# Optimization experiments

Measured on AMD Instinct MI355X. Metric: run time of the kernel, lower is better.

## Reference

```python
import jax, jax.numpy as jnp
import numpy as np

N, E, HID, H = 20000, 200000, 96, 6
HC = H * HID  # 576


def _ln(x, g, b):
    mu = x.mean(-1, keepdims=True)
    v = ((x - mu) ** 2).mean(-1, keepdims=True)
    return (x - mu) / jnp.sqrt(v + 1e-5) * g + b


def _gatv2(x, edge_emb, src, dst, Wl, bl, Wr, br, We, attw, cbias):
    # PyG GATv2Conv, concat=False, edge_dim=HID, eval mode (no dropout)
    xl = (x @ Wl + bl).reshape(N, H, HID)   # source transform (lin_l)
    xr = (x @ Wr + br).reshape(N, H, HID)   # target transform (lin_r)
    ee = (edge_emb @ We).reshape(E, H, HID) # lin_edge (no bias in PyG)
    h = jax.nn.leaky_relu(xl[src] + xr[dst] + ee, 0.2)   # [E,H,C]
    logits = jnp.einsum('ehc,hc->eh', h, attw)            # [E,H]
    m = jax.ops.segment_max(logits, dst, num_segments=N)  # segment softmax over dst
    ex = jnp.exp(logits - m[dst])
    den = jax.ops.segment_sum(ex, dst, num_segments=N)
    alpha = ex / (den[dst] + 1e-16)
    out = jax.ops.segment_sum(xl[src] * alpha[..., None], dst, num_segments=N)  # [N,H,C]
    return out.mean(axis=1) + cbias  # concat=False -> head mean, then bias


def _forward(x, edge_attr, ne_w, ne_b, ne_g, ne_beta, ee_w, ee_b, ee_g, ee_beta,
             Wl, bl, Wr, br, We, attw, cbias, lng, lnb,
             p1_w, p1_b, p1_g, p1_beta, p2_w, p2_b, p2_g, p2_beta, p3_w, p3_b,
             edge_index):
    src, dst = edge_index[0], edge_index[1]
    x = jax.nn.relu(_ln(x @ ne_w + ne_b, ne_g, ne_beta))
    edge_emb = jax.nn.relu(_ln(edge_attr @ ee_w + ee_b, ee_g, ee_beta))
    for i in range(3):  # fixed small layer count
        h = _gatv2(x, edge_emb, src, dst, Wl[i], bl[i], Wr[i], br[i], We[i], attw[i], cbias[i])
        if i < 2:
            h = jax.nn.elu(h)
        x = x + _ln(h, lng[i], lnb[i])
    ctx = jnp.concatenate([x[src], x[dst], edge_emb], axis=1)  # [E, 3*HID]
    h = jax.nn.relu(_ln(ctx @ p1_w + p1_b, p1_g, p1_beta))
    h = jax.nn.relu(_ln(h @ p2_w + p2_b, p2_g, p2_beta))
    return h @ p3_w + p3_b  # [E,1]


def setup_inputs():
    key = jax.random.key(0)
    ks = jax.random.split(key, 16)
    g = lambda k, shape, s: jax.random.normal(k, shape, dtype=jnp.float32) * s
    inp = {}
    inp['x'] = g(ks[0], (N, 4), 1.0)
    inp['edge_attr'] = g(ks[1], (E, 3), 1.0)
    inp['edge_index'] = jax.random.randint(ks[2], (2, E), 0, N, dtype=jnp.int32)
    # encoders
    inp['ne_w'] = g(ks[3], (4, HID), 0.5); inp['ne_b'] = jnp.zeros((HID,), jnp.float32)
    inp['ne_g'] = jnp.ones((HID,), jnp.float32); inp['ne_beta'] = jnp.zeros((HID,), jnp.float32)
    inp['ee_w'] = g(ks[4], (3, HID), 0.5); inp['ee_b'] = jnp.zeros((HID,), jnp.float32)
    inp['ee_g'] = jnp.ones((HID,), jnp.float32); inp['ee_beta'] = jnp.zeros((HID,), jnp.float32)
    # 3 stacked GATv2 layers
    inp['Wl'] = g(ks[5], (3, HID, HC), 0.1); inp['bl'] = jnp.zeros((3, HC), jnp.float32)
    inp['Wr'] = g(ks[6], (3, HID, HC), 0.1); inp['br'] = jnp.zeros((3, HC), jnp.float32)
    inp['We'] = g(ks[7], (3, HID, HC), 0.1)
    inp['attw'] = g(ks[8], (3, H, HID), 0.1)
    inp['cbias'] = jnp.zeros((3, HID), jnp.float32)
    inp['lng'] = jnp.ones((3, HID), jnp.float32); inp['lnb'] = jnp.zeros((3, HID), jnp.float32)
    # predictor MLP
    inp['p1_w'] = g(ks[9], (3 * HID, 128), 0.1); inp['p1_b'] = jnp.zeros((128,), jnp.float32)
    inp['p1_g'] = jnp.ones((128,), jnp.float32); inp['p1_beta'] = jnp.zeros((128,), jnp.float32)
    inp['p2_w'] = g(ks[10], (128, 64), 0.1); inp['p2_b'] = jnp.zeros((64,), jnp.float32)
    inp['p2_g'] = jnp.ones((64,), jnp.float32); inp['p2_beta'] = jnp.zeros((64,), jnp.float32)
    inp['p3_w'] = g(ks[11], (64, 1), 0.1); inp['p3_b'] = jnp.zeros((1,), jnp.float32)
    return inp


def reference(x, edge_attr, edge_index, ne_w, ne_b, ne_g, ne_beta, ee_w, ee_b, ee_g, ee_beta,
              Wl, bl, Wr, br, We, attw, cbias, lng, lnb,
              p1_w, p1_b, p1_g, p1_beta, p2_w, p2_b, p2_g, p2_beta, p3_w, p3_b):
    return _forward(x, edge_attr, ne_w, ne_b, ne_g, ne_beta, ee_w, ee_b, ee_g, ee_beta,
                    Wl, bl, Wr, br, We, attw, cbias, lng, lnb,
                    p1_w, p1_b, p1_g, p1_beta, p2_w, p2_b, p2_g, p2_beta, p3_w, p3_b,
                    edge_index)
```

## Files before the change

kernel.cpp:

```cpp
#include <hip/hip_runtime.h>
#include <math.h>

#define NN 20000
#define NE 200000

typedef __attribute__((ext_vector_type(8))) short bf16x8;
typedef __attribute__((ext_vector_type(8))) unsigned short u16x8;
typedef __attribute__((ext_vector_type(4))) float f32x4;

__device__ __forceinline__ unsigned short f2bf(float x) {
  union { float f; unsigned u; } c; c.f = x;
  unsigned r = c.u + 0x7FFF + ((c.u >> 16) & 1);
  return (unsigned short)(r >> 16);
}
__device__ __forceinline__ float bf2f(unsigned short u) {
  union { unsigned u; float f; } c; c.u = ((unsigned)u) << 16;
  return c.f;
}

template <int D>
__global__ __launch_bounds__(256) void encode_row_kernel(
    const float* __restrict__ in,
    const float* __restrict__ W, const float* __restrict__ b,
    const float* __restrict__ g, const float* __restrict__ beta,
    float* __restrict__ out, unsigned short* __restrict__ outb, int R) {
  int row = blockIdx.x * 256 + threadIdx.x;
  if (row >= R) return;
  float vin[D];
#pragma unroll
  for (int k = 0; k < D; k++) vin[k] = in[(size_t)row * D + k];
  float y[96];
  float s = 0.f, s2 = 0.f;
#pragma unroll
  for (int j = 0; j < 96; j++) {
    float v = b[j];
#pragma unroll
    for (int k = 0; k < D; k++) v += vin[k] * W[k * 96 + j];
    y[j] = v;
    s += v;
    s2 += v * v;
  }
  float mu = s * (1.f / 96.f);
  float var = s2 * (1.f / 96.f) - mu * mu;
  float rs = rsqrtf(var + 1e-5f);
#pragma unroll
  for (int c = 0; c < 12; c++) {
    u16x8 pk;
    float yo[8];
#pragma unroll
    for (int j = 0; j < 8; j++) {
      int jj = c * 8 + j;
      float v = (y[jj] - mu) * rs * g[jj] + beta[jj];
      v = fmaxf(v, 0.f);
      yo[j] = v;
      pk[j] = f2bf(v);
    }
    *(u16x8*)&outb[(size_t)row * 96 + c * 8] = pk;
    if (out) {
      f32x4 o0 = {yo[0], yo[1], yo[2], yo[3]};
      f32x4 o1 = {yo[4], yo[5], yo[6], yo[7]};
      *(f32x4*)&out[(size_t)row * 96 + c * 8] = o0;
      *(f32x4*)&out[(size_t)row * 96 + c * 8 + 4] = o1;
    }
  }
}

__global__ void convW_kernel(const float* __restrict__ We,
                             unsigned short* __restrict__ WeTb,
                             const float* __restrict__ Wl,
                             unsigned short* __restrict__ WlTb,
                             const float* __restrict__ Wr,
                             unsigned short* __restrict__ WrTb,
                             const float* __restrict__ p1w,
                             unsigned short* __restrict__ p1wT,
                             const float* __restrict__ p2w,
                             unsigned short* __restrict__ p2wT) {
  int idx = blockIdx.x * 256 + threadIdx.x;
  if (idx < 3 * 576 * 96) {
    int l = idx / (576 * 96);
    int rem = idx % (576 * 96);
    int n = rem / 96, k = rem % 96;
    size_t sidx = (size_t)l * 96 * 576 + (size_t)k * 576 + n;
    WeTb[idx] = f2bf(We[sidx]);
    WlTb[idx] = f2bf(Wl[sidx]);
    WrTb[idx] = f2bf(Wr[sidx]);
  }
  if (idx < 128 * 288) {
    int n = idx / 288, k = idx % 288;
    p1wT[idx] = f2bf(p1w[(size_t)k * 128 + n]);
  }
  if (idx < 64 * 128) {
    int n = idx / 128, k = idx % 128;
    p2wT[idx] = f2bf(p2w[(size_t)k * 64 + n]);
  }
}

__global__ void hist_kernel(const int* __restrict__ dst, int* __restrict__ deg) {
  int e = blockIdx.x * blockDim.x + threadIdx.x;
  if (e < NE) atomicAdd(&deg[dst[e]], 1);
}

__global__ __launch_bounds__(1024) void scan_kernel(
    const int* __restrict__ deg, int* __restrict__ rowptr, int* __restrict__ cursor) {
  __shared__ int wsum[16];
  int t = threadIdx.x;
  int base = t * 20;
  int loc[20];
  int s = 0;
#pragma unroll
  for (int j = 0; j < 20; j++) {
    int idx = base + j;
    int v = (idx < NN) ? deg[idx] : 0;
    loc[j] = s;
    s += v;
  }
  int lane = t & 63, wv = t >> 6;
  int inc = s;
#pragma unroll
  for (int off = 1; off < 64; off <<= 1) {
    int up = __shfl_up(inc, off);
    if (lane >= off) inc += up;
  }
  if (lane == 63) wsum[wv] = inc;
  __syncthreads();
  if (wv == 0) {
    int wval = (lane < 16) ? wsum[lane] : 0;
#pragma unroll
    for (int off = 1; off < 16; off <<= 1) {
      int up = __shfl_up(wval, off);
      if (lane >= off) wval += up;
    }
    if (lane < 16) wsum[lane] = wval;
  }
  __syncthreads();
  int wbase = (wv > 0) ? wsum[wv - 1] : 0;
  int excl = wbase + inc - s;
#pragma unroll
  for (int j = 0; j < 20; j++) {
    int idx = base + j;
    if (idx < NN) { rowptr[idx] = excl + loc[j]; cursor[idx] = excl + loc[j]; }
  }
  if (t == 0) rowptr[NN] = NE;
}

__global__ void scatter_kernel(const int* __restrict__ src,
                               const int* __restrict__ dst,
                               int* __restrict__ cursor, int* __restrict__ eidx,
                               int* __restrict__ srcp, int* __restrict__ dstp) {
  int e = blockIdx.x * blockDim.x + threadIdx.x;
  if (e < NE) {
    int d = dst[e];
    int p = atomicAdd(&cursor[d], 1);
    eidx[p] = e;
    srcp[p] = src[e];
    dstp[p] = d;
  }
}

__global__ __launch_bounds__(256) void xlxr_mfma_kernel(
    const unsigned short* __restrict__ Xb,
    const unsigned short* __restrict__ WlTb,
    const float* __restrict__ bl,
    const unsigned short* __restrict__ WrTb,
    const float* __restrict__ br,
    unsigned short* __restrict__ xlb, unsigned short* __restrict__ xrb) {
  int t = threadIdx.x;
  int wave = t >> 6, lane = t & 63;
  int l15 = lane & 15, quad = lane >> 4;
  int node = blockIdx.x * 64 + wave * 16 + l15;
  int nclamp = (node < NN) ? node : (NN - 1);
  bool valid = node < NN;
  const unsigned short* brow = &Xb[(size_t)nclamp * 96 + quad * 8];
  bf16x8 b0 = *(const bf16x8*)&brow[0];
  bf16x8 b1 = *(const bf16x8*)&brow[32];
  bf16x8 b2 = *(const bf16x8*)&brow[64];
#pragma unroll
  for (int mt = 0; mt < 36; mt++) {
    int wc = mt * 16 + l15;
    const unsigned short* aL = &WlTb[(size_t)wc * 96 + quad * 8];
    f32x4 accL = {0.f, 0.f, 0.f, 0.f};
    accL = __builtin_amdgcn_mfma_f32_16x16x32_bf16(*(const bf16x8*)&aL[0], b0, accL, 0, 0, 0);
    accL = __builtin_amdgcn_mfma_f32_16x16x32_bf16(*(const bf16x8*)&aL[32], b1, accL, 0, 0, 0);
    accL = __builtin_amdgcn_mfma_f32_16x16x32_bf16(*(const bf16x8*)&aL[64], b2, accL, 0, 0, 0);
    const unsigned short* aR = &WrTb[(size_t)wc * 96 + quad * 8];
    f32x4 accR = {0.f, 0.f, 0.f, 0.f};
    accR = __builtin_amdgcn_mfma_f32_16x16x32_bf16(*(const bf16x8*)&aR[0], b0, accR, 0, 0, 0);
    accR = __builtin_amdgcn_mfma_f32_16x16x32_bf16(*(const bf16x8*)&aR[32], b1, accR, 0, 0, 0);
    accR = __builtin_amdgcn_mfma_f32_16x16x32_bf16(*(const bf16x8*)&aR[64], b2, accR, 0, 0, 0);
    if (valid) {
      int c0 = mt * 16 + quad * 4;
      float4 bbL = *(const float4*)&bl[c0];
      float4 bbR = *(const float4*)&br[c0];
      ushort4 pL, pR;
      pL.x = f2bf(accL[0] + bbL.x); pL.y = f2bf(accL[1] + bbL.y);
      pL.z = f2bf(accL[2] + bbL.z); pL.w = f2bf(accL[3] + bbL.w);
      pR.x = f2bf(accR[0] + bbR.x); pR.y = f2bf(accR[1] + bbR.y);
      pR.z = f2bf(accR[2] + bbR.z); pR.w = f2bf(accR[3] + bbR.w);
      *(ushort4*)&xlb[(size_t)node * 576 + c0] = pL;
      *(ushort4*)&xrb[(size_t)node * 576 + c0] = pR;
    }
  }
}

__global__ __launch_bounds__(256) void logits_mfma_kernel(
    const unsigned short* __restrict__ EMBb,
    const unsigned short* __restrict__ WeTb,
    const float* __restrict__ attw,
    const unsigned short* __restrict__ XLb,
    const unsigned short* __restrict__ XRb,
    const int* __restrict__ eidx, const int* __restrict__ srcp,
    const int* __restrict__ dstp,
    float* __restrict__ logp) {
  __shared__ __align__(16) unsigned short emb[64][104];
  __shared__ __align__(16) unsigned short eeb[64][200];
  __shared__ int sd[64][2];
  int t = threadIdx.x;
  int p0 = blockIdx.x * 64;
  if (t < 128) sd[t >> 1][t & 1] = (t & 1) ? dstp[p0 + (t >> 1)] : srcp[p0 + (t >> 1)];
  {
    int e = t >> 2, c0 = (t & 3) * 24;
    int erow = eidx[p0 + e];
    const unsigned short* sp = &EMBb[(size_t)erow * 96 + c0];
    *(bf16x8*)&emb[e][c0]      = *(const bf16x8*)&sp[0];
    *(bf16x8*)&emb[e][c0 + 8]  = *(const bf16x8*)&sp[8];
    *(bf16x8*)&emb[e][c0 + 16] = *(const bf16x8*)&sp[16];
  }
  __syncthreads();

  int wave = t >> 6, lane = t & 63;
  int l15 = lane & 15, quad = lane >> 4;
  int el = t >> 2;
  int cq = (t & 3) * 24;
  int gsrc = sd[el][0];
  int gdst = sd[el][1];

  for (int hp = 0; hp < 3; hp++) {
    int h0 = hp * 2, h1 = hp * 2 + 1;
    const unsigned short* xl0 = &XLb[(size_t)gsrc * 576 + h0 * 96 + cq];
    const unsigned short* xr0 = &XRb[(size_t)gdst * 576 + h0 * 96 + cq];
    const unsigned short* xl1 = &XLb[(size_t)gsrc * 576 + h1 * 96 + cq];
    const unsigned short* xr1 = &XRb[(size_t)gdst * 576 + h1 * 96 + cq];
    bf16x8 gl0[3], gr0[3], gl1[3], gr1[3];
#pragma unroll
    for (int c8 = 0; c8 < 3; c8++) {
      gl0[c8] = *(const bf16x8*)&xl0[c8 * 8];
      gr0[c8] = *(const bf16x8*)&xr0[c8 * 8];
      gl1[c8] = *(const bf16x8*)&xl1[c8 * 8];
      gr1[c8] = *(const bf16x8*)&xr1[c8 * 8];
    }
#pragma unroll
    for (int k = 0; k < 3; k++) {
      int ntg = wave * 3 + k;
      int col = hp * 192 + ntg * 16 + l15;
      const unsigned short* brow = &WeTb[(size_t)col * 96 + quad * 8];
      bf16x8 b0 = *(const bf16x8*)&brow[0];
      bf16x8 b1 = *(const bf16x8*)&brow[32];
      bf16x8 b2 = *(const bf16x8*)&brow[64];
#pragma unroll
      for (int et = 0; et < 4; et++) {
        const unsigned short* ar = &emb[et * 16 + l15][quad * 8];
        bf16x8 a0 = *(const bf16x8*)&ar[0];
        bf16x8 a1 = *(const bf16x8*)&ar[32];
        bf16x8 a2 = *(const bf16x8*)&ar[64];
        f32x4 acc = {0.f, 0.f, 0.f, 0.f};
        acc = __builtin_amdgcn_mfma_f32_16x16x32_bf16(a0, b0, acc, 0, 0, 0);
        acc = __builtin_amdgcn_mfma_f32_16x16x32_bf16(a1, b1, acc, 0, 0, 0);
        acc = __builtin_amdgcn_mfma_f32_16x16x32_bf16(a2, b2, acc, 0, 0, 0);
#pragma unroll
        for (int r = 0; r < 4; r++)
          eeb[et * 16 + quad * 4 + r][ntg * 16 + l15] = f2bf(acc[r]);
      }
    }
    __syncthreads();
    float pl0 = 0.f, pl1 = 0.f;
    {
      const unsigned short* ee0 = &eeb[el][cq];
      const unsigned short* ee1 = &eeb[el][96 + cq];
      const f32x4* ap0 = (const f32x4*)&attw[h0 * 96 + cq];
      const f32x4* ap1 = (const f32x4*)&attw[h1 * 96 + cq];
#pragma unroll
      for (int c8 = 0; c8 < 3; c8++) {
        bf16x8 ev0 = *(const bf16x8*)&ee0[c8 * 8];
        bf16x8 ev1 = *(const bf16x8*)&ee1[c8 * 8];
        f32x4 a00 = ap0[c8 * 2], a01 = ap0[c8 * 2 + 1];
        f32x4 a10 = ap1[c8 * 2], a11 = ap1[c8 * 2 + 1];
#pragma unroll
        for (int j = 0; j < 4; j++) {
          float v0 = bf2f((unsigned short)ev0[j]) +
                     bf2f((unsigned short)gl0[c8][j]) +
                     bf2f((unsigned short)gr0[c8][j]);
          v0 = (v0 > 0.f) ? v0 : 0.2f * v0;
          pl0 += v0 * a00[j];
          float w0 = bf2f((unsigned short)ev0[j + 4]) +
                     bf2f((unsigned short)gl0[c8][j + 4]) +
                     bf2f((unsigned short)gr0[c8][j + 4]);
          w0 = (w0 > 0.f) ? w0 : 0.2f * w0;
          pl0 += w0 * a01[j];
          float v1 = bf2f((unsigned short)ev1[j]) +
                     bf2f((unsigned short)gl1[c8][j]) +
                     bf2f((unsigned short)gr1[c8][j]);
          v1 = (v1 > 0.f) ? v1 : 0.2f * v1;
          pl1 += v1 * a10[j];
          float w1 = bf2f((unsigned short)ev1[j + 4]) +
                     bf2f((unsigned short)gl1[c8][j + 4]) +
                     bf2f((unsigned short)gr1[c8][j + 4]);
          w1 = (w1 > 0.f) ? w1 : 0.2f * w1;
          pl1 += w1 * a11[j];
        }
      }
    }
    pl0 += __shfl_xor(pl0, 1); pl0 += __shfl_xor(pl0, 2);
    pl1 += __shfl_xor(pl1, 1); pl1 += __shfl_xor(pl1, 2);
    if ((t & 3) == 0) {
      size_t base = (size_t)(p0 + el) * 6 + hp * 2;
      logp[base] = pl0;
      logp[base + 1] = pl1;
    }
    __syncthreads();
  }
}

__global__ __launch_bounds__(256) void alpha_kernel(
    const float* __restrict__ logp, const int* __restrict__ rowptr,
    float* __restrict__ alpha) {
  int node = blockIdx.x * 4 + (threadIdx.x >> 6);
  int lane = threadIdx.x & 63;
  if (node >= NN) return;
  int r0 = rowptr[node], r1 = rowptr[node + 1];
  int d = r1 - r0;
  if (d == 0) return;
  if (d <= 64) {
    bool act = lane < d;
    int p = r0 + (act ? lane : (d - 1));
    float lg[6];
#pragma unroll
    for (int h = 0; h < 6; h++) lg[h] = logp[(size_t)p * 6 + h];
#pragma unroll
    for (int h = 0; h < 6; h++) {
      float m = act ? lg[h] : -1e30f;
#pragma unroll
      for (int off = 32; off > 0; off >>= 1) m = fmaxf(m, __shfl_xor(m, off));
      float w = act ? expf(lg[h] - m) : 0.f;
      float s = w;
#pragma unroll
      for (int off = 32; off > 0; off >>= 1) s += __shfl_xor(s, off);
      if (act) alpha[(size_t)p * 6 + h] = w / (s + 1e-16f);
    }
  } else {
    float m[6], s[6];
#pragma unroll
    for (int h = 0; h < 6; h++) { m[h] = -1e30f; s[h] = 0.f; }
    for (int cs = 0; cs < d; cs += 64) {
      int cnt = min(64, d - cs);
      bool act = lane < cnt;
      int p = r0 + cs + (act ? lane : (cnt - 1));
#pragma unroll
      for (int h = 0; h < 6; h++) {
        float lg = act ? logp[(size_t)p * 6 + h] : -1e30f;
        float cm = lg;
#pragma unroll
        for (int off = 32; off > 0; off >>= 1) cm = fmaxf(cm, __shfl_xor(cm, off));
        float newm = fmaxf(m[h], cm);
        float w = act ? expf(lg - newm) : 0.f;
        float ss = w;
#pragma unroll
        for (int off = 32; off > 0; off >>= 1) ss += __shfl_xor(ss, off);
        s[h] = s[h] * expf(m[h] - newm) + ss;
        m[h] = newm;
      }
    }
    float inv[6];
#pragma unroll
    for (int h = 0; h < 6; h++) inv[h] = 1.f / (s[h] + 1e-16f);
    for (int cs = 0; cs < d; cs += 64) {
      int cnt = min(64, d - cs);
      if (lane < cnt) {
        int p = r0 + cs + lane;
#pragma unroll
        for (int h = 0; h < 6; h++)
          alpha[(size_t)p * 6 + h] =
              expf(logp[(size_t)p * 6 + h] - m[h]) * inv[h];
      }
    }
  }
}

__global__ __launch_bounds__(576) void aggregate_kernel(
    float* __restrict__ x, unsigned short* __restrict__ xb,
    const unsigned short* __restrict__ XLb,
    const float* __restrict__ alpha, const int* __restrict__ rowptr,
    const int* __restrict__ srcp,
    const float* __restrict__ cbias, const float* __restrict__ lng,
    const float* __restrict__ lnb, int do_elu) {
  int n = blockIdx.x;
  int t = threadIdx.x;
  int r0 = rowptr[n];
  int d = rowptr[n + 1] - r0;
  __shared__ float scratch[576];
  __shared__ float fin[96];
  __shared__ float part[2][2];
  __shared__ float red[2];
  int wave = t >> 6, lane = t & 63;
  int h = t / 96;
  float acc = 0.f;
  int j = 0;
  for (; j + 4 <= d; j += 4) {
    int p = r0 + j;
    float w0 = alpha[(size_t)(p + 0) * 6 + h];
    float w1 = alpha[(size_t)(p + 1) * 6 + h];
    float w2 = alpha[(size_t)(p + 2) * 6 + h];
    float w3 = alpha[(size_t)(p + 3) * 6 + h];
    int s0 = srcp[p + 0], s1 = srcp[p + 1];
    int s2 = srcp[p + 2], s3 = srcp[p + 3];
    float x0 = bf2f(XLb[(size_t)s0 * 576 + t]);
    float x1 = bf2f(XLb[(size_t)s1 * 576 + t]);
    float x2 = bf2f(XLb[(size_t)s2 * 576 + t]);
    float x3 = bf2f(XLb[(size_t)s3 * 576 + t]);
    acc += w0 * x0 + w1 * x1 + w2 * x2 + w3 * x3;
  }
  for (; j < d; j++) {
    int p = r0 + j;
    acc += alpha[(size_t)p * 6 + h] * bf2f(XLb[(size_t)srcp[p] * 576 + t]);
  }
  scratch[t] = acc;
  __syncthreads();
  float fv = 0.f;
  if (t < 96) {
    float s = 0.f;
    for (int hh = 0; hh < 6; hh++) s += scratch[hh * 96 + t];
    s = s * (1.f / 6.f) + cbias[t];
    if (do_elu) s = (s > 0.f) ? s : expm1f(s);
    fv = s;
    fin[t] = s;
  }
  if (wave < 2) {
    float ps = (t < 96) ? fv : 0.f;
    float ps2 = (t < 96) ? fv * fv : 0.f;
#pragma unroll
    for (int off = 32; off > 0; off >>= 1) {
      ps += __shfl_xor(ps, off);
      ps2 += __shfl_xor(ps2, off);
    }
    if (lane == 0) { part[wave][0] = ps; part[wave][1] = ps2; }
  }
  __syncthreads();
  if (t == 0) {
    float s = part[0][0] + part[1][0];
    float s2 = part[0][1] + part[1][1];
    float mu = s / 96.f;
    float var = s2 / 96.f - mu * mu;
    red[0] = mu; red[1] = rsqrtf(var + 1e-5f);
  }
  __syncthreads();
  if (t < 96) {
    float y = (fin[t] - red[0]) * red[1] * lng[t] + lnb[t];
    float nv = x[(size_t)n * 96 + t] + y;
    x[(size_t)n * 96 + t] = nv;
    xb[(size_t)n * 96 + t] = f2bf(nv);
  }
}

__global__ __launch_bounds__(256) void pred_mfma_kernel(
    const unsigned short* __restrict__ Xb,
    const unsigned short* __restrict__ EMBb,
    const int* __restrict__ src, const int* __restrict__ dst,
    const unsigned short* __restrict__ p1wT,
    const float* __restrict__ p1b, const float* __restrict__ p1g,
    const float* __restrict__ p1be,
    const unsigned short* __restrict__ p2wT,
    const float* __restrict__ p2b, const float* __restrict__ p2g,
    const float* __restrict__ p2be,
    const float* __restrict__ p3w, const float* __restrict__ p3b,
    float* __restrict__ out) {
  __shared__ __align__(16) unsigned short fragB[4 * 9 * 64 * 8];
  __shared__ unsigned short h1s[4][16][136];
  int t = threadIdx.x;
  int wave = t >> 6, lane = t & 63;
  int l15 = lane & 15, quad = lane >> 4;
  int ebase = blockIdx.x * 64 + wave * 16;
  int erow = ebase + l15;
  int sN = src[erow], dN = dst[erow];

  bf16x8 A[9];
  const unsigned short* xs = &Xb[(size_t)sN * 96 + quad * 8];
  const unsigned short* xd = &Xb[(size_t)dN * 96 + quad * 8];
  const unsigned short* em = &EMBb[(size_t)erow * 96 + quad * 8];
#pragma unroll
  for (int c = 0; c < 3; c++) {
    A[c]     = *(const bf16x8*)&xs[c * 32];
    A[c + 3] = *(const bf16x8*)&xd[c * 32];
    A[c + 6] = *(const bf16x8*)&em[c * 32];
  }

  {
    bf16x8 tmp[9];
#pragma unroll
    for (int c = 0; c < 9; c++)
      tmp[c] = *(const bf16x8*)&p1wT[(size_t)(wave * 16 + l15) * 288 + c * 32 + quad * 8];
#pragma unroll
    for (int c = 0; c < 9; c++)
      *(bf16x8*)&fragB[((wave * 9 + c) * 64 + lane) * 8] = tmp[c];
  }
  __syncthreads();

  f32x4 C1[8];
#pragma unroll
  for (int nt = 0; nt < 4; nt++) {
    f32x4 acc = {0.f, 0.f, 0.f, 0.f};
#pragma unroll
    for (int c = 0; c < 9; c++) {
      bf16x8 B = *(const bf16x8*)&fragB[((nt * 9 + c) * 64 + lane) * 8];
      acc = __builtin_amdgcn_mfma_f32_16x16x32_bf16(A[c], B, acc, 0, 0, 0);
    }
    float bias = p1b[nt * 16 + l15];
    acc[0] += bias; acc[1] += bias; acc[2] += bias; acc[3] += bias;
    C1[nt] = acc;
  }
  __syncthreads();
  {
    bf16x8 tmp[9];
#pragma unroll
    for (int c = 0; c < 9; c++)
      tmp[c] = *(const bf16x8*)&p1wT[(size_t)((4 + wave) * 16 + l15) * 288 + c * 32 + quad * 8];
#pragma unroll
    for (int c = 0; c < 9; c++)
      *(bf16x8*)&fragB[((wave * 9 + c) * 64 + lane) * 8] = tmp[c];
  }
  __syncthreads();
#pragma unroll
  for (int nt = 4; nt < 8; nt++) {
    f32x4 acc = {0.f, 0.f, 0.f, 0.f};
#pragma unroll
    for (int c = 0; c < 9; c++) {
      bf16x8 B = *(const bf16x8*)&fragB[(((nt - 4) * 9 + c) * 64 + lane) * 8];
      acc = __builtin_amdgcn_mfma_f32_16x16x32_bf16(A[c], B, acc, 0, 0, 0);
    }
    float bias = p1b[nt * 16 + l15];
    acc[0] += bias; acc[1] += bias; acc[2] += bias; acc[3] += bias;
    C1[nt] = acc;
  }
  __syncthreads();
  {
    bf16x8 tmp[4];
#pragma unroll
    for (int c = 0; c < 4; c++)
      tmp[c] = *(const bf16x8*)&p2wT[(size_t)(wave * 16 + l15) * 128 + c * 32 + quad * 8];
#pragma unroll
    for (int c = 0; c < 4; c++)
      *(bf16x8*)&fragB[((wave * 4 + c) * 64 + lane) * 8] = tmp[c];
  }

  float mu1[4], rs1[4];
#pragma unroll
  for (int r = 0; r < 4; r++) {
    float s = 0.f, s2 = 0.f;
#pragma unroll
    for (int nt = 0; nt < 8; nt++) { float v = C1[nt][r]; s += v; s2 += v * v; }
    s += __shfl_xor(s, 1);  s += __shfl_xor(s, 2);
    s += __shfl_xor(s, 4);  s += __shfl_xor(s, 8);
    s2 += __shfl_xor(s2, 1); s2 += __shfl_xor(s2, 2);
    s2 += __shfl_xor(s2, 4); s2 += __shfl_xor(s2, 8);
    float mu = s * (1.f / 128.f);
    float var = s2 * (1.f / 128.f) - mu * mu;
    mu1[r] = mu;
    rs1[r] = rsqrtf(var + 1e-5f);
  }
#pragma unroll
  for (int nt = 0; nt < 8; nt++) {
    float g = p1g[nt * 16 + l15], be = p1be[nt * 16 + l15];
#pragma unroll
    for (int r = 0; r < 4; r++) {
      float v = (C1[nt][r] - mu1[r]) * rs1[r] * g + be;
      v = fmaxf(v, 0.f);
      h1s[wave][quad * 4 + r][nt * 16 + l15] = f2bf(v);
    }
  }
  __syncthreads();

  f32x4 C2[4];
#pragma unroll
  for (int nt = 0; nt < 4; nt++) {
    f32x4 acc = {0.f, 0.f, 0.f, 0.f};
#pragma unroll
    for (int c = 0; c < 4; c++) {
      bf16x8 Af = *(const bf16x8*)&h1s[wave][l15][c * 32 + quad * 8];
      bf16x8 B = *(const bf16x8*)&fragB[((nt * 4 + c) * 64 + lane) * 8];
      acc = __builtin_amdgcn_mfma_f32_16x16x32_bf16(Af, B, acc, 0, 0, 0);
    }
    float bias = p2b[nt * 16 + l15];
    acc[0] += bias; acc[1] += bias; acc[2] += bias; acc[3] += bias;
    C2[nt] = acc;
  }

  float mu2[4], rs2[4];
#pragma unroll
  for (int r = 0; r < 4; r++) {
    float s = 0.f, s2 = 0.f;
#pragma unroll
    for (int nt = 0; nt < 4; nt++) { float v = C2[nt][r]; s += v; s2 += v * v; }
    s += __shfl_xor(s, 1);  s += __shfl_xor(s, 2);
    s += __shfl_xor(s, 4);  s += __shfl_xor(s, 8);
    s2 += __shfl_xor(s2, 1); s2 += __shfl_xor(s2, 2);
    s2 += __shfl_xor(s2, 4); s2 += __shfl_xor(s2, 8);
    float mu = s * (1.f / 64.f);
    float var = s2 * (1.f / 64.f) - mu * mu;
    mu2[r] = mu;
    rs2[r] = rsqrtf(var + 1e-5f);
  }

  float partial[4] = {0.f, 0.f, 0.f, 0.f};
#pragma unroll
  for (int nt = 0; nt < 4; nt++) {
    float g = p2g[nt * 16 + l15], be = p2be[nt * 16 + l15];
    float pw = p3w[nt * 16 + l15];
#pragma unroll
    for (int r = 0; r < 4; r++) {
      float v = (C2[nt][r] - mu2[r]) * rs2[r] * g + be;
      v = fmaxf(v, 0.f);
      partial[r] += v * pw;
    }
  }
#pragma unroll
  for (int r = 0; r < 4; r++) {
    float p = partial[r];
    p += __shfl_xor(p, 1);
    p += __shfl_xor(p, 2);
    p += __shfl_xor(p, 4);
    p += __shfl_xor(p, 8);
    partial[r] = p;
  }
  if (l15 == 0) {
    float b3 = p3b[0];
#pragma unroll
    for (int r = 0; r < 4; r++)
      out[ebase + quad * 4 + r] = partial[r] + b3;
  }
}

static inline size_t alignup(size_t v) { return (v + 255) & ~(size_t)255; }

extern "C" void kernel_launch(void* const* d_in, const int* in_sizes, int n_in,
                              void* d_out, int out_size, void* d_ws, size_t ws_size,
                              hipStream_t stream) {
  const float* x_in      = (const float*)d_in[0];
  const float* edge_attr = (const float*)d_in[1];
  const int*   ei        = (const int*)d_in[2];
  const int* src = ei;
  const int* dst = ei + NE;
  const float* ne_w = (const float*)d_in[3];
  const float* ne_b = (const float*)d_in[4];
  const float* ne_g = (const float*)d_in[5];
  const float* ne_be = (const float*)d_in[6];
  const float* ee_w = (const float*)d_in[7];
  const float* ee_b = (const float*)d_in[8];
  const float* ee_g = (const float*)d_in[9];
  const float* ee_be = (const float*)d_in[10];
  const float* Wl = (const float*)d_in[11];
  const float* bl = (const float*)d_in[12];
  const float* Wr = (const float*)d_in[13];
  const float* br = (const float*)d_in[14];
  const float* We = (const float*)d_in[15];
  const float* attw = (const float*)d_in[16];
  const float* cbias = (const float*)d_in[17];
  const float* lng = (const float*)d_in[18];
  const float* lnb = (const float*)d_in[19];
  const float* p1w = (const float*)d_in[20];
  const float* p1b = (const float*)d_in[21];
  const float* p1g = (const float*)d_in[22];
  const float* p1be = (const float*)d_in[23];
  const float* p2w = (const float*)d_in[24];
  const float* p2b = (const float*)d_in[25];
  const float* p2g = (const float*)d_in[26];
  const float* p2be = (const float*)d_in[27];
  const float* p3w = (const float*)d_in[28];
  const float* p3b = (const float*)d_in[29];
  float* out = (float*)d_out;

  char* w = (char*)d_ws;
  float* X    = (float*)w; w += alignup((size_t)NN * 96 * 4);
  float* LOG  = (float*)w; w += alignup((size_t)NE * 6 * 4);
  float* ALPHA = (float*)w; w += alignup((size_t)NE * 6 * 4);
  unsigned short* EMBb = (unsigned short*)w; w += alignup((size_t)NE * 96 * 2);
  unsigned short* XLb  = (unsigned short*)w; w += alignup((size_t)NN * 576 * 2);
  unsigned short* XRb  = (unsigned short*)w; w += alignup((size_t)NN * 576 * 2);
  unsigned short* Xb   = (unsigned short*)w; w += alignup((size_t)NN * 96 * 2);
  unsigned short* WeTb = (unsigned short*)w; w += alignup((size_t)3 * 576 * 96 * 2);
  unsigned short* WlTb = (unsigned short*)w; w += alignup((size_t)3 * 576 * 96 * 2);
  unsigned short* WrTb = (unsigned short*)w; w += alignup((size_t)3 * 576 * 96 * 2);
  unsigned short* p1wT = (unsigned short*)w; w += alignup((size_t)128 * 288 * 2);
  unsigned short* p2wT = (unsigned short*)w; w += alignup((size_t)64 * 128 * 2);
  int* deg    = (int*)w; w += alignup((size_t)(NN + 1) * 4);
  int* rowptr = (int*)w; w += alignup((size_t)(NN + 1) * 4);
  int* cursor = (int*)w; w += alignup((size_t)NN * 4);
  int* eidx   = (int*)w; w += alignup((size_t)NE * 4);
  int* srcp   = (int*)w; w += alignup((size_t)NE * 4);
  int* dstp   = (int*)w; w += alignup((size_t)NE * 4);

  encode_row_kernel<4><<<(NN + 255) / 256, 256, 0, stream>>>(
      x_in, ne_w, ne_b, ne_g, ne_be, X, Xb, NN);
  encode_row_kernel<3><<<(NE + 255) / 256, 256, 0, stream>>>(
      edge_attr, ee_w, ee_b, ee_g, ee_be, nullptr, EMBb, NE);
  convW_kernel<<<(3 * 576 * 96 + 255) / 256, 256, 0, stream>>>(
      We, WeTb, Wl, WlTb, Wr, WrTb, p1w, p1wT, p2w, p2wT);

  hipMemsetAsync(deg, 0, (size_t)(NN + 1) * 4, stream);
  hist_kernel<<<(NE + 255) / 256, 256, 0, stream>>>(dst, deg);
  scan_kernel<<<1, 1024, 0, stream>>>(deg, rowptr, cursor);
  scatter_kernel<<<(NE + 255) / 256, 256, 0, stream>>>(src, dst, cursor, eidx,
                                                       srcp, dstp);

  for (int i = 0; i < 3; i++) {
    const unsigned short* WlT_i = WlTb + (size_t)i * 576 * 96;
    const float* bl_i = bl + (size_t)i * 576;
    const unsigned short* WrT_i = WrTb + (size_t)i * 576 * 96;
    const float* br_i = br + (size_t)i * 576;
    const unsigned short* WeT_i = WeTb + (size_t)i * 576 * 96;
    const float* aw_i = attw + (size_t)i * 576;
    const float* cb_i = cbias + (size_t)i * 96;
    const float* lg_i = lng + (size_t)i * 96;
    const float* lb_i = lnb + (size_t)i * 96;
    xlxr_mfma_kernel<<<(NN + 63) / 64, 256, 0, stream>>>(Xb, WlT_i, bl_i,
                                                         WrT_i, br_i, XLb, XRb);
    logits_mfma_kernel<<<NE / 64, 256, 0, stream>>>(EMBb, WeT_i, aw_i, XLb, XRb,
                                                    eidx, srcp, dstp, LOG);
    alpha_kernel<<<(NN + 3) / 4, 256, 0, stream>>>(LOG, rowptr, ALPHA);
    aggregate_kernel<<<NN, 576, 0, stream>>>(X, Xb, XLb, ALPHA, rowptr, srcp,
                                             cb_i, lg_i, lb_i, (i < 2) ? 1 : 0);
  }

  pred_mfma_kernel<<<NE / 64, 256, 0, stream>>>(Xb, EMBb, src, dst,
                                                p1wT, p1b, p1g, p1be,
                                                p2wT, p2b, p2g, p2be,
                                                p3w, p3b, out);
}
```

Baseline: 984.9 us.

## Vectorize aggregate gather with 16-byte loads and split edges across thread slots

The aggregation kernel now has each thread load 8 bf16 channels of a source row with one 16-byte load instead of one scalar per thread. The 576 threads are split into 8 edge slots that each process a strided subset of the destination's neighbors, followed by a shared-memory reduction across slots. Source indices and alpha values are staged in shared memory in chunks of 64 edges. This cuts per-edge load instructions and redundant alpha/index reads, but adds extra barriers and a reduction step, and nodes with low degree may leave many slots idle.

```diff
diff --git a/kernel.cpp b/kernel.cpp
--- a/kernel.cpp
+++ b/kernel.cpp
@@ -396,38 +396,53 @@
   int t = threadIdx.x;
   int r0 = rowptr[n];
   int d = rowptr[n + 1] - r0;
-  __shared__ float scratch[576];
+  __shared__ float scratch[8][584];
+  __shared__ int sdv[64];
+  __shared__ float av[64][6];
   __shared__ float fin[96];
   __shared__ float part[2][2];
   __shared__ float red[2];
   int wave = t >> 6, lane = t & 63;
-  int h = t / 96;
-  float acc = 0.f;
-  int j = 0;
-  for (; j + 4 <= d; j += 4) {
-    int p = r0 + j;
-    float w0 = alpha[(size_t)(p + 0) * 6 + h];
-    float w1 = alpha[(size_t)(p + 1) * 6 + h];
-    float w2 = alpha[(size_t)(p + 2) * 6 + h];
-    float w3 = alpha[(size_t)(p + 3) * 6 + h];
-    int s0 = srcp[p + 0], s1 = srcp[p + 1];
-    int s2 = srcp[p + 2], s3 = srcp[p + 3];
-    float x0 = bf2f(XLb[(size_t)s0 * 576 + t]);
-    float x1 = bf2f(XLb[(size_t)s1 * 576 + t]);
-    float x2 = bf2f(XLb[(size_t)s2 * 576 + t]);
-    float x3 = bf2f(XLb[(size_t)s3 * 576 + t]);
-    acc += w0 * x0 + w1 * x1 + w2 * x2 + w3 * x3;
-  }
-  for (; j < d; j++) {
-    int p = r0 + j;
-    acc += alpha[(size_t)p * 6 + h] * bf2f(XLb[(size_t)srcp[p] * 576 + t]);
-  }
-  scratch[t] = acc;
+  int slot = t / 72;
+  int c8 = t % 72;
+  int ch = c8 * 8;
+  int h = ch / 96;
+  float acc[8] = {0.f, 0.f, 0.f, 0.f, 0.f, 0.f, 0.f, 0.f};
+
+  for (int base = 0; base < d; base += 64) {
+    int cnt = min(64, d - base);
+    if (base > 0) __syncthreads();
+    if (t < cnt) sdv[t] = srcp[r0 + base + t];
+    if (t >= 64 && t < 64 + cnt * 6) {
+      int u = t - 64;
+      av[u / 6][u % 6] = alpha[(size_t)(r0 + base + u / 6) * 6 + (u % 6)];
+    }
+    __syncthreads();
+    for (int j = slot; j < cnt; j += 8) {
+      float w = av[j][h];
+      int s = sdv[j];
+      bf16x8 xv = *(const bf16x8*)&XLb[(size_t)s * 576 + ch];
+#pragma unroll
+      for (int q = 0; q < 8; q++) acc[q] += w * bf2f((unsigned short)xv[q]);
+    }
+  }
+  f32x4 a0 = {acc[0], acc[1], acc[2], acc[3]};
+  f32x4 a1 = {acc[4], acc[5], acc[6], acc[7]};
+  *(f32x4*)&scratch[slot][ch] = a0;
+  *(f32x4*)&scratch[slot][ch + 4] = a1;
+  __syncthreads();
+  {
+    float v = 0.f;
+#pragma unroll
+    for (int sl = 0; sl < 8; sl++) v += scratch[sl][t];
+    __syncthreads();
+    scratch[0][t] = v;
+  }
   __syncthreads();
   float fv = 0.f;
   if (t < 96) {
     float s = 0.f;
-    for (int hh = 0; hh < 6; hh++) s += scratch[hh * 96 + t];
+    for (int hh = 0; hh < 6; hh++) s += scratch[0][hh * 96 + t];
     s = s * (1.f / 6.f) + cbias[t];
     if (do_elu) s = (s > 0.f) ? s : expm1f(s);
     fv = s;
```

Measured after the change: 1.075 ms. +9.2%, slower.

## Aggregate six nodes per block with each thread summing all heads for one channel

Applied to the files above, without the earlier changes.

The aggregate kernel used to map one node to a 576-thread block, one thread per head-channel, followed by a cross-head reduction in shared memory. It now processes six nodes per block, one 96-thread group per node, and each thread accumulates all six heads for its channel in registers. That removes the shared-memory head reduction and one barrier, and each warp computes one node's layernorm statistics. The cost is six strided 2-byte gathers per edge per thread in place of one coalesced load, and nodes with very different degrees now share a block, which can cause load imbalance within it.

```diff
diff --git a/kernel.cpp b/kernel.cpp
--- a/kernel.cpp
+++ b/kernel.cpp
@@ -392,71 +392,82 @@
     const int* __restrict__ srcp,
     const float* __restrict__ cbias, const float* __restrict__ lng,
     const float* __restrict__ lnb, int do_elu) {
-  int n = blockIdx.x;
   int t = threadIdx.x;
-  int r0 = rowptr[n];
-  int d = rowptr[n + 1] - r0;
-  __shared__ float scratch[576];
-  __shared__ float fin[96];
-  __shared__ float part[2][2];
-  __shared__ float red[2];
+  int nb = t / 96, c = t % 96;
+  int n = blockIdx.x * 6 + nb;
+  bool vn = (n < NN);
+  __shared__ float fin[6][96];
+  __shared__ float red[6][2];
   int wave = t >> 6, lane = t & 63;
-  int h = t / 96;
+  int r0 = 0, d = 0;
+  if (vn) { r0 = rowptr[n]; d = rowptr[n + 1] - r0; }
   float acc = 0.f;
   int j = 0;
-  for (; j + 4 <= d; j += 4) {
+  for (; j + 1 < d; j += 2) {
     int p = r0 + j;
-    float w0 = alpha[(size_t)(p + 0) * 6 + h];
-    float w1 = alpha[(size_t)(p + 1) * 6 + h];
-    float w2 = alpha[(size_t)(p + 2) * 6 + h];
-    float w3 = alpha[(size_t)(p + 3) * 6 + h];
-    int s0 = srcp[p + 0], s1 = srcp[p + 1];
-    int s2 = srcp[p + 2], s3 = srcp[p + 3];
-    float x0 = bf2f(XLb[(size_t)s0 * 576 + t]);
-    float x1 = bf2f(XLb[(size_t)s1 * 576 + t]);
-    float x2 = bf2f(XLb[(size_t)s2 * 576 + t]);
-    float x3 = bf2f(XLb[(size_t)s3 * 576 + t]);
-    acc += w0 * x0 + w1 * x1 + w2 * x2 + w3 * x3;
-  }
-  for (; j < d; j++) {
+    int s0 = srcp[p], s1 = srcp[p + 1];
+    const float* ap0 = &alpha[(size_t)p * 6];
+    float2 a00 = *(const float2*)&ap0[0];
+    float2 a01 = *(const float2*)&ap0[2];
+    float2 a02 = *(const float2*)&ap0[4];
+    float2 a10 = *(const float2*)&ap0[6];
+    float2 a11 = *(const float2*)&ap0[8];
+    float2 a12 = *(const float2*)&ap0[10];
+    const unsigned short* xp0 = &XLb[(size_t)s0 * 576 + c];
+    const unsigned short* xp1 = &XLb[(size_t)s1 * 576 + c];
+    unsigned short v00 = xp0[0],   v01 = xp0[96],  v02 = xp0[192];
+    unsigned short v03 = xp0[288], v04 = xp0[384], v05 = xp0[480];
+    unsigned short v10 = xp1[0],   v11 = xp1[96],  v12 = xp1[192];
+    unsigned short v13 = xp1[288], v14 = xp1[384], v15 = xp1[480];
+    acc += a00.x * bf2f(v00) + a00.y * bf2f(v01) + a01.x * bf2f(v02) +
+           a01.y * bf2f(v03) + a02.x * bf2f(v04) + a02.y * bf2f(v05);
+    acc += a10.x * bf2f(v10) + a10.y * bf2f(v11) + a11.x * bf2f(v12) +
+           a11.y * bf2f(v13) + a12.x * bf2f(v14) + a12.y * bf2f(v15);
+  }
+  if (j < d) {
     int p = r0 + j;
-    acc += alpha[(size_t)p * 6 + h] * bf2f(XLb[(size_t)srcp[p] * 576 + t]);
-  }
-  scratch[t] = acc;
-  __syncthreads();
+    int s0 = srcp[p];
+    const float* ap0 = &alpha[(size_t)p * 6];
+    float2 a00 = *(const float2*)&ap0[0];
+    float2 a01 = *(const float2*)&ap0[2];
+    float2 a02 = *(const float2*)&ap0[4];
+    const unsigned short* xp0 = &XLb[(size_t)s0 * 576 + c];
+    unsigned short v00 = xp0[0],   v01 = xp0[96],  v02 = xp0[192];
+    unsigned short v03 = xp0[288], v04 = xp0[384], v05 = xp0[480];
+    acc += a00.x * bf2f(v00) + a00.y * bf2f(v01) + a01.x * bf2f(v02) +
+           a01.y * bf2f(v03) + a02.x * bf2f(v04) + a02.y * bf2f(v05);
+  }
   float fv = 0.f;
-  if (t < 96) {
-    float s = 0.f;
-    for (int hh = 0; hh < 6; hh++) s += scratch[hh * 96 + t];
-    s = s * (1.f / 6.f) + cbias[t];
+  if (vn) {
+    float s = acc * (1.f / 6.f) + cbias[c];
     if (do_elu) s = (s > 0.f) ? s : expm1f(s);
     fv = s;
-    fin[t] = s;
-  }
-  if (wave < 2) {
-    float ps = (t < 96) ? fv : 0.f;
-    float ps2 = (t < 96) ? fv * fv : 0.f;
+  }
+  fin[nb][c] = fv;
+  __syncthreads();
+  if (wave < 6) {
+    float x0 = fin[wave][lane];
+    float x1 = (lane < 32) ? fin[wave][64 + lane] : 0.f;
+    float s = x0 + x1;
+    float s2 = x0 * x0 + x1 * x1;
 #pragma unroll
     for (int off = 32; off > 0; off >>= 1) {
-      ps += __shfl_xor(ps, off);
-      ps2 += __shfl_xor(ps2, off);
-    }
-    if (lane == 0) { part[wave][0] = ps; part[wave][1] = ps2; }
-  }
-  __syncthreads();
-  if (t == 0) {
-    float s = part[0][0] + part[1][0];
-    float s2 = part[0][1] + part[1][1];
-    float mu = s / 96.f;
-    float var = s2 / 96.f - mu * mu;
-    red[0] = mu; red[1] = rsqrtf(var + 1e-5f);
-  }
-  __syncthreads();
-  if (t < 96) {
-    float y = (fin[t] - red[0]) * red[1] * lng[t] + lnb[t];
-    float nv = x[(size_t)n * 96 + t] + y;
-    x[(size_t)n * 96 + t] = nv;
-    xb[(size_t)n * 96 + t] = f2bf(nv);
+      s += __shfl_xor(s, off);
+      s2 += __shfl_xor(s2, off);
+    }
+    if (lane == 0) {
+      float mu = s * (1.f / 96.f);
+      float var = s2 * (1.f / 96.f) - mu * mu;
+      red[wave][0] = mu;
+      red[wave][1] = rsqrtf(var + 1e-5f);
+    }
+  }
+  __syncthreads();
+  if (vn) {
+    float y = (fv - red[nb][0]) * red[nb][1] * lng[c] + lnb[c];
+    float nv = x[(size_t)n * 96 + c] + y;
+    x[(size_t)n * 96 + c] = nv;
+    xb[(size_t)n * 96 + c] = f2bf(nv);
   }
 }
 
@@ -724,8 +735,10 @@
     logits_mfma_kernel<<<NE / 64, 256, 0, stream>>>(EMBb, WeT_i, aw_i, XLb, XRb,
                                                     eidx, srcp, dstp, LOG);
     alpha_kernel<<<(NN + 3) / 4, 256, 0, stream>>>(LOG, rowptr, ALPHA);
-    aggregate_kernel<<<NN, 576, 0, stream>>>(X, Xb, XLb, ALPHA, rowptr, srcp,
-                                             cb_i, lg_i, lb_i, (i < 2) ? 1 : 0);
+    aggregate_kernel<<<(NN + 5) / 6, 576, 0, stream>>>(X, Xb, XLb, ALPHA,
+                                                       rowptr, srcp,
+                                                       cb_i, lg_i, lb_i,
+                                                       (i < 2) ? 1 : 0);
   }
 
   pred_mfma_kernel<<<NE / 64, 256, 0, stream>>>(Xb, EMBb, src, dst,
```

Result: faster. 864.6 us (-12.2%).
